# Performance work log

Hardware: AMD Instinct MI355X
Metric: run time of the kernel (lower is better)

Reference implementation:

```python
import jax, jax.numpy as jnp
import numpy as np


def setup_inputs() -> dict:
    key = jax.random.key(0)
    B, N, C = 8, 8192, 256
    z = jax.random.normal(key, (B, N, C), dtype=jnp.float32)
    return {"z": z, "width": 9}


def reference(z, width):
    # activation='exp'
    a = jnp.exp(z)                      # (B, N, C)
    # conv1d with all-ones (C,C,width) kernel == width-window sliding sum of the
    # per-position channel-sum, broadcast back over channels.
    s = jnp.sum(a, axis=-1)             # (B, N)
    half = width // 2
    p = jnp.pad(s, ((0, 0), (half, half)))          # (B, N + width - 1)
    c = jnp.pad(jnp.cumsum(p, axis=1), ((0, 0), (1, 0)))  # (B, N + width)
    denom = c[:, width:] - c[:, :-width]            # (B, N) windowed sum
    return z * a / denom[..., None]
```

## Files before the change

kernel.cpp:

```cpp
#include <hip/hip_runtime.h>


static constexpr int kB   = 8;
static constexpr int kN   = 8192;
static constexpr int kC   = 256;
static constexpr int ROWS = 64;
static constexpr int HALO = 4;
static constexpr int THREADS = 512;
static constexpr int RPW  = 8;

__global__ void __launch_bounds__(THREADS)
fused_spatial_softmax(const float* __restrict__ z, const int* __restrict__ wptr,
                      float* __restrict__ out) {
    __shared__ float s_lds[ROWS + 2 * HALO];

    const int wave = threadIdx.x >> 6;
    const int lane = threadIdx.x & 63;
    const int blocksPerBatch = kN / ROWS;
    const int b  = blockIdx.x / blocksPerBatch;
    const int n0 = (blockIdx.x % blocksPerBatch) * ROWS;

    const float* zb = z   + ((size_t)b * kN + n0) * kC;
    float*       ob = out + ((size_t)b * kN + n0) * kC;

    const int r0 = wave * RPW;
    float4 v[RPW];
#pragma unroll
    for (int i = 0; i < RPW; ++i)
        v[i] = reinterpret_cast<const float4*>(zb + (size_t)(r0 + i) * kC)[lane];

    {
        const int nrel = (wave < HALO) ? (wave - HALO) : (ROWS + wave - HALO);
        const int n = n0 + nrel;
        float e = 0.0f;
        if (n >= 0 && n < kN) {
            const float4 hv = reinterpret_cast<const float4*>(
                z + ((size_t)b * kN + n) * kC)[lane];
            e = __expf(hv.x) + __expf(hv.y) + __expf(hv.z) + __expf(hv.w);
#pragma unroll
            for (int off = 32; off >= 1; off >>= 1) e += __shfl_xor(e, off);
        }
        if (lane == 0) s_lds[HALO + nrel] = e;
    }

#pragma unroll
    for (int i = 0; i < RPW; ++i) {
        float e = __expf(v[i].x) + __expf(v[i].y) + __expf(v[i].z) + __expf(v[i].w);
#pragma unroll
        for (int off = 32; off >= 1; off >>= 1) e += __shfl_xor(e, off);
        if (lane == 0) s_lds[HALO + r0 + i] = e;
    }

    __syncthreads();

    const int width = *wptr;
    const int half  = width >> 1;

#pragma unroll
    for (int i = 0; i < RPW; ++i) {
        const int nrel = r0 + i;
        float d = 0.0f;
        const int base = HALO + nrel - half;
        for (int k = 0; k < width; ++k) d += s_lds[base + k];
        const float rinv = 1.0f / d;
        float4 o;
        o.x = v[i].x * __expf(v[i].x) * rinv;
        o.y = v[i].y * __expf(v[i].y) * rinv;
        o.z = v[i].z * __expf(v[i].z) * rinv;
        o.w = v[i].w * __expf(v[i].w) * rinv;
        reinterpret_cast<float4*>(ob + (size_t)nrel * kC)[lane] = o;
    }
}

extern "C" void kernel_launch(void* const* d_in, const int* in_sizes, int n_in,
                              void* d_out, int out_size, void* d_ws, size_t ws_size,
                              hipStream_t stream) {
    const float* z    = (const float*)d_in[0];
    const int*   wptr = (const int*)d_in[1];
    float*       out  = (float*)d_out;

    const int blocks = (kB * kN) / ROWS;
    fused_spatial_softmax<<<blocks, THREADS, 0, stream>>>(z, wptr, out);
}
```

Measured before the change: 29.85 us.

## Enlarge blocks, cache z*exp(z), use rcp and nontemporal stores

Doubles rows per block to 128 with 1024 threads, so each block still loads only 8 halo rows while covering more output rows. Each exp is computed once: z*exp(z) is kept in registers instead of being recomputed after the barrier. The exact division becomes the hardware approximate reciprocal, and output stores use nontemporal hints to avoid polluting cache. Loads are now interleaved with the exp and reduction work rather than all issued up front, which may reduce memory-level parallelism, and the reciprocal loses a little precision.

```diff
diff --git a/kernel.cpp b/kernel.cpp
--- a/kernel.cpp
+++ b/kernel.cpp
@@ -1,13 +1,16 @@
 #include <hip/hip_runtime.h>
 
 
-static constexpr int kB   = 8;
-static constexpr int kN   = 8192;
-static constexpr int kC   = 256;
-static constexpr int ROWS = 64;
-static constexpr int HALO = 4;
-static constexpr int THREADS = 512;
-static constexpr int RPW  = 8;
+typedef float f32x4 __attribute__((ext_vector_type(4)));
+
+static constexpr int kB      = 8;
+static constexpr int kN      = 8192;
+static constexpr int kC      = 256;
+static constexpr int ROWS    = 128;
+static constexpr int HALO    = 4;
+static constexpr int THREADS = 1024;
+static constexpr int WAVES   = THREADS / 64;
+static constexpr int RPW     = ROWS / WAVES;
 
 __global__ void __launch_bounds__(THREADS)
 fused_spatial_softmax(const float* __restrict__ z, const int* __restrict__ wptr,
@@ -20,21 +23,20 @@
     const int b  = blockIdx.x / blocksPerBatch;
     const int n0 = (blockIdx.x % blocksPerBatch) * ROWS;
 
+    const int width = *wptr;
+    const int half  = width >> 1;
+
     const float* zb = z   + ((size_t)b * kN + n0) * kC;
     float*       ob = out + ((size_t)b * kN + n0) * kC;
 
     const int r0 = wave * RPW;
-    float4 v[RPW];
-#pragma unroll
-    for (int i = 0; i < RPW; ++i)
-        v[i] = reinterpret_cast<const float4*>(zb + (size_t)(r0 + i) * kC)[lane];
 
-    {
+    if (wave < 2 * HALO) {
         const int nrel = (wave < HALO) ? (wave - HALO) : (ROWS + wave - HALO);
         const int n = n0 + nrel;
         float e = 0.0f;
         if (n >= 0 && n < kN) {
-            const float4 hv = reinterpret_cast<const float4*>(
+            const f32x4 hv = reinterpret_cast<const f32x4*>(
                 z + ((size_t)b * kN + n) * kC)[lane];
             e = __expf(hv.x) + __expf(hv.y) + __expf(hv.z) + __expf(hv.w);
 #pragma unroll
@@ -43,18 +45,25 @@
         if (lane == 0) s_lds[HALO + nrel] = e;
     }
 
+    f32x4 w[RPW];
 #pragma unroll
     for (int i = 0; i < RPW; ++i) {
-        float e = __expf(v[i].x) + __expf(v[i].y) + __expf(v[i].z) + __expf(v[i].w);
+        const f32x4 v = reinterpret_cast<const f32x4*>(zb + (size_t)(r0 + i) * kC)[lane];
+        const float ex = __expf(v.x);
+        const float ey = __expf(v.y);
+        const float ez = __expf(v.z);
+        const float ew = __expf(v.w);
+        float e = ex + ey + ez + ew;
 #pragma unroll
         for (int off = 32; off >= 1; off >>= 1) e += __shfl_xor(e, off);
         if (lane == 0) s_lds[HALO + r0 + i] = e;
+        w[i].x = v.x * ex;
+        w[i].y = v.y * ey;
+        w[i].z = v.z * ez;
+        w[i].w = v.w * ew;
     }
 
     __syncthreads();
-
-    const int width = *wptr;
-    const int half  = width >> 1;
 
 #pragma unroll
     for (int i = 0; i < RPW; ++i) {
@@ -62,13 +71,14 @@
         float d = 0.0f;
         const int base = HALO + nrel - half;
         for (int k = 0; k < width; ++k) d += s_lds[base + k];
-        const float rinv = 1.0f / d;
-        float4 o;
-        o.x = v[i].x * __expf(v[i].x) * rinv;
-        o.y = v[i].y * __expf(v[i].y) * rinv;
-        o.z = v[i].z * __expf(v[i].z) * rinv;
-        o.w = v[i].w * __expf(v[i].w) * rinv;
-        reinterpret_cast<float4*>(ob + (size_t)nrel * kC)[lane] = o;
+        const float rinv = __builtin_amdgcn_rcpf(d);
+        f32x4 o;
+        o.x = w[i].x * rinv;
+        o.y = w[i].y * rinv;
+        o.z = w[i].z * rinv;
+        o.w = w[i].w * rinv;
+        __builtin_nontemporal_store(o,
+            reinterpret_cast<f32x4*>(ob + (size_t)nrel * kC) + lane);
     }
 }
 
```

New measurement: 29.43 us. No clear change (-1.4%).
